# Kernel tuning notes

Hardware: AMD Instinct MI355X
Metric: run time of the kernel (lower is better)

## Reference

```python
import jax, jax.numpy as jnp
import numpy as np

B, H, W, C = 2, 48, 96, 128
N = H * W
NH, HD = 8, 32
WIN_R = 1
WLEN = 2 * WIN_R + 2
ATTN_NUM = WLEN * WLEN
FIELD_DIM = 2
D_SELF = C + FIELD_DIM + NH * 2   # 146
E_SELF = D_SELF + 1               # 147 (noc embed)
D_CROSS = C + FIELD_DIM           # 130
ATTN_DIM = NH * HD                # 256
HID = C * 2                       # ConvGLU hidden
SCALE = HD ** -0.5


def init_coords():
    gx, gy = jnp.meshgrid(jnp.arange(W, dtype=jnp.float32), jnp.arange(H, dtype=jnp.float32))
    return jnp.stack([gx, gy], axis=-1)[None]  # [1,H,W,2] (x,y)


def layer_norm(x, g, b, eps=1e-5):
    mu = x.mean(-1, keepdims=True)
    var = ((x - mu) ** 2).mean(-1, keepdims=True)
    return (x - mu) * jax.lax.rsqrt(var + eps) * g + b


def swap_halves(t):
    a, b = jnp.split(t, 2, axis=0)
    return jnp.concatenate([b, a], axis=0)


def bilinear_sample(img, coords):
    # img [B,H,W,C]; coords [B,H,W,2] absolute (x,y)
    x = jnp.clip(coords[..., 0], 0.0, W - 1.0)
    y = jnp.clip(coords[..., 1], 0.0, H - 1.0)
    x0 = jnp.clip(jnp.floor(x), 0, W - 2).astype(jnp.int32); x1 = x0 + 1
    y0 = jnp.clip(jnp.floor(y), 0, H - 2).astype(jnp.int32); y1 = y0 + 1
    wx = (x - x0)[..., None]; wy = (y - y0)[..., None]
    bi = jnp.arange(img.shape[0])[:, None, None]
    v00 = img[bi, y0, x0]; v01 = img[bi, y0, x1]
    v10 = img[bi, y1, x0]; v11 = img[bi, y1, x1]
    return (1 - wy) * ((1 - wx) * v00 + wx * v01) + wy * ((1 - wx) * v10 + wx * v11)


def consistency_mask(field, A=2.0):
    offset = field + init_coords()
    f_t2r = bilinear_sample(swap_halves(field), offset)
    diff = jnp.abs(field + f_t2r).sum(-1, keepdims=True)
    return (diff < A).astype(field.dtype)  # [B,H,W,1]


def match_attention_core(q, k, v, max_offset):
    # q,k,v: [B,N,NH,HD]; max_offset: [B,N,NH,2] absolute (x,y)
    r = WIN_R
    ox = jnp.clip(max_offset[..., 0], float(r), W - 1 - r - 0.001)
    oy = jnp.clip(max_offset[..., 1], float(r), H - 1 - r - 0.001)
    mxf = jnp.floor(ox); myf = jnp.floor(oy)
    fx = (ox - mxf).transpose(0, 2, 1)[..., None, None]  # [B,NH,N,1,1]
    fy = (oy - myf).transpose(0, 2, 1)[..., None, None]
    mx = mxf.astype(jnp.int32).transpose(0, 2, 1)  # [B,NH,N]
    my = myf.astype(jnp.int32).transpose(0, 2, 1)
    qh = q.transpose(0, 2, 1, 3); kh = k.transpose(0, 2, 1, 3); vh = v.transpose(0, 2, 1, 3)
    dxs = jnp.arange(WLEN) - r                    # window: floor-r .. floor+r+1
    gx = mx[..., None] + dxs                      # [B,NH,N,WLEN]
    gy = my[..., None] + dxs
    idx = (gy[..., :, None] * W + gx[..., None, :]).reshape(B, NH, N, ATTN_NUM)
    bi = jnp.arange(B)[:, None, None, None]
    hi = jnp.arange(NH)[None, :, None, None]
    kg = kh[bi, hi, idx]                          # [B,NH,N,ATTN_NUM,HD]
    s = jnp.einsum('bhnd,bhnad->bhna', qh, kg) * SCALE
    S = s.reshape(B, NH, N, WLEN, WLEN)           # [..., y, x]
    w00 = (1 - fy) * (1 - fx); w01 = (1 - fy) * fx; w10 = fy * (1 - fx); w11 = fy * fx
    # continuous (2r+1)^2 window scores by bilinear interp of integer-grid scores
    s_cont = (w00 * S[..., :-1, :-1] + w01 * S[..., :-1, 1:]
              + w10 * S[..., 1:, :-1] + w11 * S[..., 1:, 1:])
    p = jax.nn.softmax(s_cont.reshape(B, NH, N, -1), axis=-1).reshape(s_cont.shape)
    # scatter continuous probs back to the (2r+2)^2 integer grid with bilinear weights
    Ag = jnp.zeros((B, NH, N, WLEN, WLEN), p.dtype)
    Ag = Ag.at[..., :-1, :-1].add(w00 * p)
    Ag = Ag.at[..., :-1, 1:].add(w01 * p)
    Ag = Ag.at[..., 1:, :-1].add(w10 * p)
    Ag = Ag.at[..., 1:, 1:].add(w11 * p)
    Af = Ag.reshape(B, NH, N, ATTN_NUM)
    vg = vh[bi, hi, idx]                          # [B,NH,N,ATTN_NUM,HD]
    out = jnp.einsum('bhna,bhnad->bhnd', Af, vg)
    return out.transpose(0, 2, 1, 3).reshape(B, N, ATTN_DIM), Af.transpose(0, 2, 1, 3)


def reference(x, self_rpos, field, field_scale, n0_g, n0_b, n1_g, n1_b, n2_g, n2_b,
              sq_w, sk_w, sv_w, sp_w, cq_w, ck_w, cv_w, cg_w, cp_w,
              fc1_w, fc1_b, dw_w, dw_b, fc2_w, fc2_b):
    noc = consistency_mask(jax.lax.stop_gradient(field))
    xc = jnp.concatenate([x, field * field_scale, self_rpos], axis=-1)  # [B,H,W,D_SELF]
    coords0 = jnp.tile(init_coords(), (1, 1, 1, NH))  # [1,H,W,2*NH]
    self_off = (self_rpos + coords0).reshape(B, N, NH, 2)
    # --- self MatchAttention (noc_embed) ---
    h0 = layer_norm(xc, n0_g, n0_b).reshape(B, N, D_SELF)
    xe = jnp.concatenate([h0, noc.reshape(B, N, 1)], axis=-1)
    q = (xe @ sq_w).reshape(B, N, NH, HD)
    k = (xe @ sk_w).reshape(B, N, NH, HD)
    v = (xe @ sv_w).reshape(B, N, NH, HD)
    o, _ = match_attention_core(q, k, v, self_off)
    xc = xc + (o @ sp_w).reshape(B, H, W, D_SELF)
    self_rpos_out = xc[..., -NH * 2:]
    xc = xc[..., :D_CROSS]
    xc = xc.at[..., -1].set(0.0)  # stereo: zero y-flow
    field1 = xc[..., -FIELD_DIM:] / field_scale
    off = (jnp.tile(field1, (1, 1, 1, NH)) + coords0).reshape(B, N, NH, 2)
    # --- cross MatchAttention ---
    h1 = layer_norm(xc, n1_g, n1_b).reshape(B, N, D_CROSS)
    ref = h1
    tgt = swap_halves(h1)
    g = jax.nn.silu(ref @ cg_w)
    q = (ref @ cq_w).reshape(B, N, NH, HD)
    k = (tgt @ ck_w).reshape(B, N, NH, HD)
    v = (tgt @ cv_w).reshape(B, N, NH, HD)
    o, attn = match_attention_core(q, k, v, off)
    o = jnp.concatenate([g * o, attn.reshape(B, N, NH * ATTN_NUM)], axis=-1)
    xc = xc + (o @ cp_w).reshape(B, H, W, D_CROSS)
    xc = xc.at[..., -1].set(0.0)
    field2 = xc[..., -FIELD_DIM:] / field_scale
    xo = xc[..., :C]
    # --- ConvGLU MLP ---
    h2 = layer_norm(xo, n2_g, n2_b)
    u = h2 @ fc1_w + fc1_b
    a, gv = jnp.split(u, 2, axis=-1)
    a = jax.lax.conv_general_dilated(a, dw_w, (1, 1), 'SAME',
                                     dimension_numbers=('NHWC', 'HWIO', 'NHWC'),
                                     feature_group_count=HID) + dw_b
    a = jax.nn.gelu(a, approximate=False) * gv
    xo = xo + (a @ fc2_w + fc2_b)
    return xo, self_rpos_out, field2


def setup_inputs() -> dict:
    key = jax.random.key(0)
    ks = jax.random.split(key, 16)
    def rn(i, shape, s=1.0):
        return jax.random.normal(ks[i], shape, dtype=jnp.float32) * s
    return {
        'x': rn(0, (B, H, W, C)),
        'self_rpos': rn(1, (B, H, W, NH * 2)),
        'field': rn(2, (B, H, W, FIELD_DIM)),
        'field_scale': 0.1 * jnp.ones((1, 1, 1, 2), jnp.float32),
        'n0_g': jnp.ones((D_SELF,), jnp.float32), 'n0_b': jnp.zeros((D_SELF,), jnp.float32),
        'n1_g': jnp.ones((D_CROSS,), jnp.float32), 'n1_b': jnp.zeros((D_CROSS,), jnp.float32),
        'n2_g': jnp.ones((C,), jnp.float32), 'n2_b': jnp.zeros((C,), jnp.float32),
        'sq_w': rn(3, (E_SELF, ATTN_DIM), 0.02), 'sk_w': rn(4, (E_SELF, ATTN_DIM), 0.02),
        'sv_w': rn(5, (E_SELF, ATTN_DIM), 0.02), 'sp_w': rn(6, (ATTN_DIM, D_SELF), 0.02),
        'cq_w': rn(7, (D_CROSS, ATTN_DIM), 0.02), 'ck_w': rn(8, (D_CROSS, ATTN_DIM), 0.02),
        'cv_w': rn(9, (D_CROSS, ATTN_DIM), 0.02), 'cg_w': rn(10, (D_CROSS, ATTN_DIM), 0.02),
        'cp_w': rn(11, (ATTN_DIM + NH * ATTN_NUM, D_CROSS), 0.02),
        'fc1_w': rn(12, (C, 2 * HID), 0.02), 'fc1_b': jnp.zeros((2 * HID,), jnp.float32),
        'dw_w': rn(13, (3, 3, 1, HID), 0.1), 'dw_b': jnp.zeros((HID,), jnp.float32),
        'fc2_w': rn(14, (HID, C), 0.02), 'fc2_b': jnp.zeros((C,), jnp.float32),
    }
```

## Files before the change

### kernel.cpp

```cpp
#include <hip/hip_runtime.h>
#include <math.h>

namespace {
constexpr int Bn = 2, Hh = 48, Ww = 96, Cch = 128;
constexpr int Nn = Hh * Ww;
constexpr int NHh = 8;
constexpr int DSELF = 146, ESELF = 147, DCROSS = 130;
constexpr int Mrows = Bn * Nn;
constexpr float SCALEf = 0.17677669529663687f;
}

typedef float f32x4 __attribute__((ext_vector_type(4)));
typedef short s16x8 __attribute__((ext_vector_type(8)));

__device__ __forceinline__ unsigned short f2b(float f) {
  unsigned int u = __float_as_uint(f);
  u = u + 0x7fffu + ((u >> 16) & 1u);
  return (unsigned short)(u >> 16);
}

__device__ __forceinline__ f32x4 mfma_bf16(s16x8 a, s16x8 b, f32x4 c) {
  f32x4 d;
  asm volatile("v_mfma_f32_16x16x32_bf16 %0, %1, %2, %3"
               : "=&v"(d) : "v"(a), "v"(b), "v"(c));
  return d;
}

__device__ __forceinline__ float wave_bcast_sum(float v) {
#pragma unroll
  for (int off = 32; off > 0; off >>= 1) v += __shfl_down(v, off);
  return __shfl(v, 0);
}

struct WDesc { const float* src; int K, N, Kp, dstOff, blkOff; };
struct WPack { WDesc d[11]; };

__global__ __launch_bounds__(256) void convert_w_kernel(WPack p, unsigned short* dst) {
  int bi = blockIdx.x;
  int mi = 0;
#pragma unroll
  for (int i = 1; i < 11; i++) if (bi >= p.d[i].blkOff) mi = i;
  WDesc w = p.d[mi];
  int e = (bi - w.blkOff) * 2048 + threadIdx.x * 8;
  int total = w.N * w.Kp;
  if (e >= total) return;
  int n = e / w.Kp, k0 = e - n * w.Kp;
  s16x8 pack;
#pragma unroll
  for (int j = 0; j < 8; j++) {
    int kk = k0 + j;
    float vv = (kk < w.K) ? w.src[(size_t)kk * w.N + n] : 0.f;
    pack[j] = (short)f2b(vv);
  }
  *reinterpret_cast<s16x8*>(dst + w.dstOff + e) = pack;
}

__global__ __launch_bounds__(256) void mfma_gemm_kernel(
    const unsigned short* __restrict__ A, int Kp,
    const unsigned short* __restrict__ Wt, int N,
    const float* __restrict__ bias, const float* __restrict__ resid,
    float* __restrict__ out, int swapA, int act) {
  __shared__ unsigned short As[64 * 40];
  __shared__ unsigned short Bs[64 * 40];
  int tid = threadIdx.x;
  int m0 = blockIdx.y * 64, n0 = blockIdx.x * 64;
  int lane = tid & 63, wv = tid >> 6;
  int wr = wv >> 1, wc = wv & 1;
  int lr = lane & 15, lk = (lane >> 4) * 8;
  int sr = tid >> 2, sk8 = (tid & 3) * 8;
  int am = m0 + sr;
  if (swapA) am = (am < Mrows / 2) ? am + Mrows / 2 : am - Mrows / 2;
  const unsigned short* aptr = A + (size_t)am * Kp + sk8;
  int bn = n0 + sr;
  const unsigned short* bptr = (bn < N) ? Wt + (size_t)bn * Kp + sk8 : nullptr;
  f32x4 acc00 = {}, acc01 = {}, acc10 = {}, acc11 = {};
  for (int k0 = 0; k0 < Kp; k0 += 32) {
    s16x8 av = *reinterpret_cast<const s16x8*>(aptr + k0);
    s16x8 bv = {};
    if (bptr) bv = *reinterpret_cast<const s16x8*>(bptr + k0);
    *reinterpret_cast<s16x8*>(&As[sr * 40 + sk8]) = av;
    *reinterpret_cast<s16x8*>(&Bs[sr * 40 + sk8]) = bv;
    __syncthreads();
    s16x8 a0 = *reinterpret_cast<const s16x8*>(&As[(wr * 32 + lr) * 40 + lk]);
    s16x8 a1 = *reinterpret_cast<const s16x8*>(&As[(wr * 32 + 16 + lr) * 40 + lk]);
    s16x8 b0 = *reinterpret_cast<const s16x8*>(&Bs[(wc * 32 + lr) * 40 + lk]);
    s16x8 b1 = *reinterpret_cast<const s16x8*>(&Bs[(wc * 32 + 16 + lr) * 40 + lk]);
    acc00 = mfma_bf16(a0, b0, acc00);
    acc01 = mfma_bf16(a0, b1, acc01);
    acc10 = mfma_bf16(a1, b0, acc10);
    acc11 = mfma_bf16(a1, b1, acc11);
    __syncthreads();
  }
  int rowBase = m0 + wr * 32 + (lane >> 4) * 4;
  f32x4 accs[2][2] = {{acc00, acc01}, {acc10, acc11}};
#pragma unroll
  for (int fc = 0; fc < 2; fc++) {
    int col = n0 + wc * 32 + fc * 16 + lr;
    if (col >= N) continue;
    float bval = bias ? bias[col] : 0.f;
#pragma unroll
    for (int fr = 0; fr < 2; fr++) {
#pragma unroll
      for (int r = 0; r < 4; r++) {
        int row = rowBase + fr * 16 + r;
        float vv = accs[fr][fc][r] + bval;
        if (resid) vv += resid[(size_t)row * N + col];
        if (act == 1) vv = vv / (1.f + expf(-vv));
        out[(size_t)row * N + col] = vv;
      }
    }
  }
}

__global__ __launch_bounds__(256) void prep_kernel(
    const float* __restrict__ x, const float* __restrict__ rpos,
    const float* __restrict__ field, const float* __restrict__ fs,
    const float* __restrict__ n0g, const float* __restrict__ n0b,
    float* __restrict__ xc, unsigned short* __restrict__ xe_b) {
  int wv = threadIdx.x >> 6, lane = threadIdx.x & 63;
  int pix = blockIdx.x * 4 + wv;
  int b = pix / Nn, n = pix - b * Nn;
  int py = n / Ww, px = n - py * Ww;
  const float* xrow = x + (size_t)pix * Cch;
  const float* rrow = rpos + (size_t)pix * 16;
  float f0 = field[(size_t)pix * 2 + 0], f1 = field[(size_t)pix * 2 + 1];
  float fsx = fs[0], fsy = fs[1];
  float vals[3];
#pragma unroll
  for (int i = 0; i < 3; i++) {
    int c = lane + i * 64;
    float v = 0.f;
    if (c < Cch) v = xrow[c];
    else if (c == 128) v = f0 * fsx;
    else if (c == 129) v = f1 * fsy;
    else if (c < DSELF) v = rrow[c - 130];
    vals[i] = v;
  }
  float* xcrow = xc + (size_t)pix * DSELF;
#pragma unroll
  for (int i = 0; i < 3; i++) {
    int c = lane + i * 64;
    if (c < DSELF) xcrow[c] = vals[i];
  }
  float s = 0.f;
#pragma unroll
  for (int i = 0; i < 3; i++) { int c = lane + i * 64; if (c < DSELF) s += vals[i]; }
  float mu = wave_bcast_sum(s) * (1.f / DSELF);
  float s2 = 0.f;
#pragma unroll
  for (int i = 0; i < 3; i++) {
    int c = lane + i * 64;
    if (c < DSELF) { float d = vals[i] - mu; s2 += d * d; }
  }
  float var = wave_bcast_sum(s2) * (1.f / DSELF);
  float rs = rsqrtf(var + 1e-5f);
  float noc = 0.f;
  if (lane == 0) {
    float ox = fminf(fmaxf(f0 + (float)px, 0.f), (float)(Ww - 1));
    float oy = fminf(fmaxf(f1 + (float)py, 0.f), (float)(Hh - 1));
    float x0f = fminf(fmaxf(floorf(ox), 0.f), (float)(Ww - 2));
    float y0f = fminf(fmaxf(floorf(oy), 0.f), (float)(Hh - 2));
    int x0 = (int)x0f, y0 = (int)y0f;
    float wx = ox - x0f, wy = oy - y0f;
    const float* fo = field + (size_t)(1 - b) * Nn * 2;
    const float* p00 = fo + ((size_t)y0 * Ww + x0) * 2;
    const float* p10 = fo + ((size_t)(y0 + 1) * Ww + x0) * 2;
    float v0 = (1.f - wy) * ((1.f - wx) * p00[0] + wx * p00[2]) +
               wy * ((1.f - wx) * p10[0] + wx * p10[2]);
    float v1 = (1.f - wy) * ((1.f - wx) * p00[1] + wx * p00[3]) +
               wy * ((1.f - wx) * p10[1] + wx * p10[3]);
    float diff = fabsf(f0 + v0) + fabsf(f1 + v1);
    noc = (diff < 2.f) ? 1.f : 0.f;
  }
  noc = __shfl(noc, 0);
  unsigned short* xerow = xe_b + (size_t)pix * 160;
#pragma unroll
  for (int i = 0; i < 3; i++) {
    int c = lane + i * 64;
    if (c < 160) {
      float v;
      if (c < DSELF) v = (vals[i] - mu) * rs * n0g[c] + n0b[c];
      else if (c == 146) v = noc;
      else v = 0.f;
      xerow[c] = f2b(v);
    }
  }
}

__global__ __launch_bounds__(256) void attn_wave_kernel(
    const float* __restrict__ q, const float* __restrict__ k,
    const float* __restrict__ v, const float* __restrict__ rpos,
    const float* __restrict__ xc2, const float* __restrict__ fs,
    const float* __restrict__ g, unsigned short* __restrict__ o, int o_stride,
    int mode) {
  int wv = threadIdx.x >> 6, lane = threadIdx.x & 63;
  int pix = blockIdx.x * 4 + wv;
  int b = pix / Nn, n = pix - b * Nn;
  int py = n / Ww, px = n - py * Ww;
  int h = lane >> 3, c = lane & 7;
  size_t row = (size_t)pix;
  float ox, oy;
  if (mode == 0) {
    ox = rpos[row * 16 + 2 * h] + (float)px;
    oy = rpos[row * 16 + 2 * h + 1] + (float)py;
  } else {
    ox = xc2[row * DCROSS + 128] / fs[0] + (float)px;
    oy = (float)py;
  }
  ox = fminf(fmaxf(ox, 1.0f), 93.999f);
  oy = fminf(fmaxf(oy, 1.0f), 45.999f);
  float mxf = floorf(ox), myf = floorf(oy);
  float fx = ox - mxf, fy = oy - myf;
  int mx = (int)mxf, my = (int)myf;
  int base = b * Nn;

  float4 qv = *reinterpret_cast<const float4*>(q + row * 256 + lane * 4);
  float s[16];
#pragma unroll
  for (int j = 0; j < 4; j++) {
    int gy = my - 1 + j;
#pragma unroll
    for (int i = 0; i < 4; i++) {
      int gx = mx - 1 + i;
      int idx = gy * Ww + gx;
      float4 kv = *reinterpret_cast<const float4*>(
          k + (size_t)(base + idx) * 256 + lane * 4);
      float d = qv.x * kv.x + qv.y * kv.y + qv.z * kv.z + qv.w * kv.w;
      d += __shfl_xor(d, 1);
      d += __shfl_xor(d, 2);
      d += __shfl_xor(d, 4);
      s[j * 4 + i] = d * SCALEf;
    }
  }
  float w00 = (1.f - fy) * (1.f - fx), w01 = (1.f - fy) * fx;
  float w10 = fy * (1.f - fx), w11 = fy * fx;
  float sc[9];
#pragma unroll
  for (int j = 0; j < 3; j++)
#pragma unroll
    for (int i = 0; i < 3; i++)
      sc[j * 3 + i] = w00 * s[j * 4 + i] + w01 * s[j * 4 + i + 1] +
                      w10 * s[(j + 1) * 4 + i] + w11 * s[(j + 1) * 4 + i + 1];
  float mval = sc[0];
#pragma unroll
  for (int i = 1; i < 9; i++) mval = fmaxf(mval, sc[i]);
  float p[9], psum = 0.f;
#pragma unroll
  for (int i = 0; i < 9; i++) { p[i] = expf(sc[i] - mval); psum += p[i]; }
  float inv = 1.f / psum;
#pragma unroll
  for (int i = 0; i < 9; i++) p[i] *= inv;
  float Ag[16] = {};
#pragma unroll
  for (int j = 0; j < 3; j++)
#pragma unroll
    for (int i = 0; i < 3; i++) {
      float pv = p[j * 3 + i];
      Ag[j * 4 + i] += w00 * pv;
      Ag[j * 4 + i + 1] += w01 * pv;
      Ag[(j + 1) * 4 + i] += w10 * pv;
      Ag[(j + 1) * 4 + i + 1] += w11 * pv;
    }
  float4 acc = make_float4(0.f, 0.f, 0.f, 0.f);
#pragma unroll
  for (int j = 0; j < 4; j++) {
    int gy = my - 1 + j;
#pragma unroll
    for (int i = 0; i < 4; i++) {
      int gx = mx - 1 + i;
      int idx = gy * Ww + gx;
      float4 vv = *reinterpret_cast<const float4*>(
          v + (size_t)(base + idx) * 256 + lane * 4);
      float w = Ag[j * 4 + i];
      acc.x += w * vv.x; acc.y += w * vv.y; acc.z += w * vv.z; acc.w += w * vv.w;
    }
  }
  if (g) {
    float4 gg = *reinterpret_cast<const float4*>(g + row * 256 + lane * 4);
    acc.x *= gg.x; acc.y *= gg.y; acc.z *= gg.z; acc.w *= gg.w;
  }
  unsigned int p0 = (unsigned int)f2b(acc.x) | ((unsigned int)f2b(acc.y) << 16);
  unsigned int p1 = (unsigned int)f2b(acc.z) | ((unsigned int)f2b(acc.w) << 16);
  *reinterpret_cast<uint2*>(o + row * o_stride + lane * 4) = make_uint2(p0, p1);
  if (mode == 1) {
    float a0 = 0.f, a1 = 0.f;
#pragma unroll
    for (int a = 0; a < 8; a++) {
      if (c == a) { a0 = Ag[2 * a]; a1 = Ag[2 * a + 1]; }
    }
    unsigned int pa = (unsigned int)f2b(a0) | ((unsigned int)f2b(a1) << 16);
    *reinterpret_cast<unsigned int*>(o + row * o_stride + 256 + h * 16 + 2 * c) = pa;
  }
}

__global__ __launch_bounds__(256) void post_self_kernel(
    const float* __restrict__ xcn, const float* __restrict__ n1g,
    const float* __restrict__ n1b, float* __restrict__ out_rpos,
    float* __restrict__ xc2, unsigned short* __restrict__ h1_b) {
  int wv = threadIdx.x >> 6, lane = threadIdx.x & 63;
  int pix = blockIdx.x * 4 + wv;
  const float* row = xcn + (size_t)pix * DSELF;
  float vals[3];
#pragma unroll
  for (int i = 0; i < 3; i++) {
    int c = lane + i * 64;
    vals[i] = (c < DSELF) ? row[c] : 0.f;
  }
#pragma unroll
  for (int i = 0; i < 3; i++) {
    int c = lane + i * 64;
    if (c >= 130 && c < 146) out_rpos[(size_t)pix * 16 + (c - 130)] = vals[i];
  }
#pragma unroll
  for (int i = 0; i < 3; i++) {
    int c = lane + i * 64;
    if (c == 129) vals[i] = 0.f;
  }
  float* x2row = xc2 + (size_t)pix * DCROSS;
#pragma unroll
  for (int i = 0; i < 3; i++) {
    int c = lane + i * 64;
    if (c < DCROSS) x2row[c] = vals[i];
  }
  float s = 0.f;
#pragma unroll
  for (int i = 0; i < 3; i++) { int c = lane + i * 64; if (c < DCROSS) s += vals[i]; }
  float mu = wave_bcast_sum(s) * (1.f / DCROSS);
  float s2 = 0.f;
#pragma unroll
  for (int i = 0; i < 3; i++) {
    int c = lane + i * 64;
    if (c < DCROSS) { float d = vals[i] - mu; s2 += d * d; }
  }
  float var = wave_bcast_sum(s2) * (1.f / DCROSS);
  float rs = rsqrtf(var + 1e-5f);
  unsigned short* h1row = h1_b + (size_t)pix * 160;
#pragma unroll
  for (int i = 0; i < 3; i++) {
    int c = lane + i * 64;
    if (c < 160) {
      float v = (c < DCROSS) ? (vals[i] - mu) * rs * n1g[c] + n1b[c] : 0.f;
      h1row[c] = f2b(v);
    }
  }
}

__global__ __launch_bounds__(256) void post_cross_kernel(
    const float* __restrict__ xc2n, const float* __restrict__ fs,
    const float* __restrict__ n2g, const float* __restrict__ n2b,
    float* __restrict__ out_f2, float* __restrict__ xob,
    unsigned short* __restrict__ h2_b) {
  int wv = threadIdx.x >> 6, lane = threadIdx.x & 63;
  int pix = blockIdx.x * 4 + wv;
  const float* row = xc2n + (size_t)pix * DCROSS;
  float vals[3];
#pragma unroll
  for (int i = 0; i < 3; i++) {
    int c = lane + i * 64;
    vals[i] = (c < DCROSS) ? row[c] : 0.f;
  }
  if (lane == 0) out_f2[(size_t)pix * 2 + 0] = vals[2] / fs[0];
  if (lane == 1) out_f2[(size_t)pix * 2 + 1] = 0.f;
  float* xrow = xob + (size_t)pix * Cch;
#pragma unroll
  for (int i = 0; i < 2; i++) {
    int c = lane + i * 64;
    xrow[c] = vals[i];
  }
  float s = vals[0] + vals[1];
  float mu = wave_bcast_sum(s) * (1.f / Cch);
  float d0 = vals[0] - mu, d1 = vals[1] - mu;
  float var = wave_bcast_sum(d0 * d0 + d1 * d1) * (1.f / Cch);
  float rs = rsqrtf(var + 1e-5f);
  unsigned short* h2row = h2_b + (size_t)pix * Cch;
#pragma unroll
  for (int i = 0; i < 2; i++) {
    int c = lane + i * 64;
    h2row[c] = f2b((vals[i] - mu) * rs * n2g[c] + n2b[c]);
  }
}

__global__ __launch_bounds__(256) void dwconv_kernel(
    const float* __restrict__ u, const float* __restrict__ dww,
    const float* __restrict__ dwb, unsigned short* __restrict__ aout) {
  int t = blockIdx.x * 256 + threadIdx.x;
  int c = t & 255;
  int pix = t >> 8;
  int b = pix / Nn, n = pix - b * Nn;
  int py = n / Ww, px = n - py * Ww;
  float acc = dwb[c];
#pragma unroll
  for (int ky = 0; ky < 3; ky++) {
    int yy = py + ky - 1;
    if (yy < 0 || yy >= Hh) continue;
#pragma unroll
    for (int kx = 0; kx < 3; kx++) {
      int xx = px + kx - 1;
      if (xx < 0 || xx >= Ww) continue;
      acc += u[((size_t)(b * Nn + yy * Ww + xx)) * 512 + c] * dww[(ky * 3 + kx) * 256 + c];
    }
  }
  float ge = 0.5f * acc * (1.f + erff(acc * 0.70710678118654752f));
  aout[(size_t)pix * 256 + c] = f2b(ge * u[(size_t)pix * 512 + 256 + c]);
}

extern "C" void kernel_launch(void* const* d_in, const int* in_sizes, int n_in,
                              void* d_out, int out_size, void* d_ws, size_t ws_size,
                              hipStream_t stream) {
  (void)in_sizes; (void)n_in; (void)out_size; (void)ws_size;
  const float* x    = (const float*)d_in[0];
  const float* rpos = (const float*)d_in[1];
  const float* field= (const float*)d_in[2];
  const float* fs   = (const float*)d_in[3];
  const float* n0g  = (const float*)d_in[4];
  const float* n0b  = (const float*)d_in[5];
  const float* n1g  = (const float*)d_in[6];
  const float* n1b  = (const float*)d_in[7];
  const float* n2g  = (const float*)d_in[8];
  const float* n2b  = (const float*)d_in[9];
  const float* sq_w = (const float*)d_in[10];
  const float* sk_w = (const float*)d_in[11];
  const float* sv_w = (const float*)d_in[12];
  const float* sp_w = (const float*)d_in[13];
  const float* cq_w = (const float*)d_in[14];
  const float* ck_w = (const float*)d_in[15];
  const float* cv_w = (const float*)d_in[16];
  const float* cg_w = (const float*)d_in[17];
  const float* cp_w = (const float*)d_in[18];
  const float* fc1w = (const float*)d_in[19];
  const float* fc1b = (const float*)d_in[20];
  const float* dww  = (const float*)d_in[21];
  const float* dwb  = (const float*)d_in[22];
  const float* fc2w = (const float*)d_in[23];
  const float* fc2b = (const float*)d_in[24];

  float* ws = (float*)d_ws;
  float* xc   = ws + 0;
  float* xcn  = ws + 1345536;
  float* q    = ws + 2691072;
  float* k    = ws + 5050368;
  float* v    = ws + 7409664;
  float* g    = ws + 9768960;
  float* xc2  = ws + 12128256;
  float* xob  = ws + 13326336;
  unsigned short* xe_b   = (unsigned short*)(ws + 14505984);
  unsigned short* o_b    = (unsigned short*)(ws + 15243264);
  unsigned short* h1_b   = (unsigned short*)(ws + 16422912);
  unsigned short* ocat_b = (unsigned short*)(ws + 17160192);
  unsigned short* h2_b   = (unsigned short*)(ws + 18929664);
  unsigned short* warena = (unsigned short*)(ws + 19519488);
  float* u    = q;
  float* xc2n = v;
  unsigned short* aconv_b = o_b;

  float* out_xo   = (float*)d_out;
  float* out_rpos = out_xo + 1179648;
  float* out_f2   = out_xo + 1327104;

  const int oSQ = 0, oSK = 40960, oSV = 81920, oSP = 122880, oCQ = 160256,
            oCK = 201216, oCV = 242176, oCG = 283136, oCP = 324096,
            oF1 = 374016, oF2 = 439552;
  WPack wp;
  auto setw = [&](int i, const float* src, int K, int N, int Kp, int off) {
    wp.d[i].src = src; wp.d[i].K = K; wp.d[i].N = N; wp.d[i].Kp = Kp;
    wp.d[i].dstOff = off;
  };
  setw(0, sq_w, 147, 256, 160, oSQ);
  setw(1, sk_w, 147, 256, 160, oSK);
  setw(2, sv_w, 147, 256, 160, oSV);
  setw(3, sp_w, 256, 146, 256, oSP);
  setw(4, cq_w, 130, 256, 160, oCQ);
  setw(5, ck_w, 130, 256, 160, oCK);
  setw(6, cv_w, 130, 256, 160, oCV);
  setw(7, cg_w, 130, 256, 160, oCG);
  setw(8, cp_w, 384, 130, 384, oCP);
  setw(9, fc1w, 128, 512, 128, oF1);
  setw(10, fc2w, 256, 128, 256, oF2);
  int nblk = 0;
  for (int i = 0; i < 11; i++) {
    wp.d[i].blkOff = nblk;
    nblk += (wp.d[i].N * wp.d[i].Kp + 2047) / 2048;
  }

  dim3 blk(256);
  auto gemm = [&](const unsigned short* A, int Kp, int woff, int N,
                  const float* bias, const float* resid, float* out,
                  int swapA, int act) {
    dim3 grid((N + 63) / 64, Mrows / 64);
    mfma_gemm_kernel<<<grid, blk, 0, stream>>>(A, Kp, warena + woff, N, bias,
                                               resid, out, swapA, act);
  };

  convert_w_kernel<<<nblk, blk, 0, stream>>>(wp, warena);
  prep_kernel<<<2304, blk, 0, stream>>>(x, rpos, field, fs, n0g, n0b, xc, xe_b);
  gemm(xe_b, 160, oSQ, 256, nullptr, nullptr, q, 0, 0);
  gemm(xe_b, 160, oSK, 256, nullptr, nullptr, k, 0, 0);
  gemm(xe_b, 160, oSV, 256, nullptr, nullptr, v, 0, 0);
  attn_wave_kernel<<<2304, blk, 0, stream>>>(q, k, v, rpos, nullptr, fs, nullptr,
                                             o_b, 256, 0);
  gemm(o_b, 256, oSP, 146, nullptr, xc, xcn, 0, 0);
  post_self_kernel<<<2304, blk, 0, stream>>>(xcn, n1g, n1b, out_rpos, xc2, h1_b);
  gemm(h1_b, 160, oCQ, 256, nullptr, nullptr, q, 0, 0);
  gemm(h1_b, 160, oCK, 256, nullptr, nullptr, k, 1, 0);
  gemm(h1_b, 160, oCV, 256, nullptr, nullptr, v, 1, 0);
  gemm(h1_b, 160, oCG, 256, nullptr, nullptr, g, 0, 1);
  attn_wave_kernel<<<2304, blk, 0, stream>>>(q, k, v, nullptr, xc2, fs, g,
                                             ocat_b, 384, 1);
  gemm(ocat_b, 384, oCP, 130, nullptr, xc2, xc2n, 0, 0);
  post_cross_kernel<<<2304, blk, 0, stream>>>(xc2n, fs, n2g, n2b, out_f2, xob, h2_b);
  gemm(h2_b, 128, oF1, 512, fc1b, nullptr, u, 0, 0);
  dwconv_kernel<<<9216, blk, 0, stream>>>(u, dww, dwb, aconv_b);
  gemm(aconv_b, 256, oF2, 128, fc2b, xob, out_xo, 0, 0);
}
```

Measured before the change: 182.8 us.

## Fuse QKV and cross projections into wide GEMMs, store FFN hidden as bf16

Packs the self-attention Q/K/V weights into one contiguous block and runs a single N=768 GEMM. The cross Q+G and K+V projections become two N=512 GEMMs, with SiLU applied only to the gate columns. The attention kernel now reads q/k/v/g through strides and offsets into these interleaved buffers. The fc1 output is written as bf16, and the depthwise conv is vectorised to process 8 channels per thread from that bf16 buffer. This cuts kernel launches and halves the memory traffic of the FFN intermediate, at the cost of bf16 rounding on the hidden activations and larger attention read strides.

```diff
diff --git a/kernel.cpp b/kernel.cpp
--- a/kernel.cpp
+++ b/kernel.cpp
@@ -18,6 +18,9 @@
   u = u + 0x7fffu + ((u >> 16) & 1u);
   return (unsigned short)(u >> 16);
 }
+__device__ __forceinline__ float b2f(unsigned short u) {
+  return __uint_as_float((unsigned int)u << 16);
+}
 
 __device__ __forceinline__ f32x4 mfma_bf16(s16x8 a, s16x8 b, f32x4 c) {
   f32x4 d;
@@ -59,7 +62,7 @@
     const unsigned short* __restrict__ A, int Kp,
     const unsigned short* __restrict__ Wt, int N,
     const float* __restrict__ bias, const float* __restrict__ resid,
-    float* __restrict__ out, int swapA, int act) {
+    void* __restrict__ out, int swapA, int act, int out_bf16) {
   __shared__ unsigned short As[64 * 40];
   __shared__ unsigned short Bs[64 * 40];
   int tid = threadIdx.x;
@@ -98,6 +101,7 @@
     int col = n0 + wc * 32 + fc * 16 + lr;
     if (col >= N) continue;
     float bval = bias ? bias[col] : 0.f;
+    bool dosilu = (act == 1) || (act == 2 && col >= 256);
 #pragma unroll
     for (int fr = 0; fr < 2; fr++) {
 #pragma unroll
@@ -105,8 +109,11 @@
         int row = rowBase + fr * 16 + r;
         float vv = accs[fr][fc][r] + bval;
         if (resid) vv += resid[(size_t)row * N + col];
-        if (act == 1) vv = vv / (1.f + expf(-vv));
-        out[(size_t)row * N + col] = vv;
+        if (dosilu) vv = vv / (1.f + expf(-vv));
+        if (out_bf16)
+          ((unsigned short*)out)[(size_t)row * N + col] = f2b(vv);
+        else
+          ((float*)out)[(size_t)row * N + col] = vv;
       }
     }
   }
@@ -188,10 +195,10 @@
 }
 
 __global__ __launch_bounds__(256) void attn_wave_kernel(
-    const float* __restrict__ q, const float* __restrict__ k,
-    const float* __restrict__ v, const float* __restrict__ rpos,
-    const float* __restrict__ xc2, const float* __restrict__ fs,
-    const float* __restrict__ g, unsigned short* __restrict__ o, int o_stride,
+    const float* __restrict__ qbuf, int qstride, int gOff,
+    const float* __restrict__ kvbuf, int kvstride, int koff, int voff,
+    const float* __restrict__ rpos, const float* __restrict__ xc2,
+    const float* __restrict__ fs, unsigned short* __restrict__ o, int o_stride,
     int mode) {
   int wv = threadIdx.x >> 6, lane = threadIdx.x & 63;
   int pix = blockIdx.x * 4 + wv;
@@ -214,7 +221,7 @@
   int mx = (int)mxf, my = (int)myf;
   int base = b * Nn;
 
-  float4 qv = *reinterpret_cast<const float4*>(q + row * 256 + lane * 4);
+  float4 qv = *reinterpret_cast<const float4*>(qbuf + row * qstride + lane * 4);
   float s[16];
 #pragma unroll
   for (int j = 0; j < 4; j++) {
@@ -224,7 +231,7 @@
       int gx = mx - 1 + i;
       int idx = gy * Ww + gx;
       float4 kv = *reinterpret_cast<const float4*>(
-          k + (size_t)(base + idx) * 256 + lane * 4);
+          kvbuf + (size_t)(base + idx) * kvstride + koff + lane * 4);
       float d = qv.x * kv.x + qv.y * kv.y + qv.z * kv.z + qv.w * kv.w;
       d += __shfl_xor(d, 1);
       d += __shfl_xor(d, 2);
@@ -270,13 +277,13 @@
       int gx = mx - 1 + i;
       int idx = gy * Ww + gx;
       float4 vv = *reinterpret_cast<const float4*>(
-          v + (size_t)(base + idx) * 256 + lane * 4);
+          kvbuf + (size_t)(base + idx) * kvstride + voff + lane * 4);
       float w = Ag[j * 4 + i];
       acc.x += w * vv.x; acc.y += w * vv.y; acc.z += w * vv.z; acc.w += w * vv.w;
     }
   }
-  if (g) {
-    float4 gg = *reinterpret_cast<const float4*>(g + row * 256 + lane * 4);
+  if (gOff >= 0) {
+    float4 gg = *reinterpret_cast<const float4*>(qbuf + row * qstride + gOff + lane * 4);
     acc.x *= gg.x; acc.y *= gg.y; acc.z *= gg.z; acc.w *= gg.w;
   }
   unsigned int p0 = (unsigned int)f2b(acc.x) | ((unsigned int)f2b(acc.y) << 16);
@@ -381,14 +388,16 @@
 }
 
 __global__ __launch_bounds__(256) void dwconv_kernel(
-    const float* __restrict__ u, const float* __restrict__ dww,
+    const unsigned short* __restrict__ ub, const float* __restrict__ dww,
     const float* __restrict__ dwb, unsigned short* __restrict__ aout) {
   int t = blockIdx.x * 256 + threadIdx.x;
-  int c = t & 255;
-  int pix = t >> 8;
+  int c8 = (t & 31) * 8;
+  int pix = t >> 5;
   int b = pix / Nn, n = pix - b * Nn;
   int py = n / Ww, px = n - py * Ww;
-  float acc = dwb[c];
+  float acc[8];
+#pragma unroll
+  for (int j = 0; j < 8; j++) acc[j] = dwb[c8 + j];
 #pragma unroll
   for (int ky = 0; ky < 3; ky++) {
     int yy = py + ky - 1;
@@ -397,11 +406,23 @@
     for (int kx = 0; kx < 3; kx++) {
       int xx = px + kx - 1;
       if (xx < 0 || xx >= Ww) continue;
-      acc += u[((size_t)(b * Nn + yy * Ww + xx)) * 512 + c] * dww[(ky * 3 + kx) * 256 + c];
-    }
-  }
-  float ge = 0.5f * acc * (1.f + erff(acc * 0.70710678118654752f));
-  aout[(size_t)pix * 256 + c] = f2b(ge * u[(size_t)pix * 512 + 256 + c]);
+      s16x8 uv = *reinterpret_cast<const s16x8*>(
+          ub + ((size_t)(b * Nn + yy * Ww + xx)) * 512 + c8);
+      const float* wrow = dww + (ky * 3 + kx) * 256 + c8;
+#pragma unroll
+      for (int j = 0; j < 8; j++)
+        acc[j] += b2f((unsigned short)uv[j]) * wrow[j];
+    }
+  }
+  s16x8 gate = *reinterpret_cast<const s16x8*>(ub + (size_t)pix * 512 + 256 + c8);
+  s16x8 outp;
+#pragma unroll
+  for (int j = 0; j < 8; j++) {
+    float a = acc[j];
+    float ge = 0.5f * a * (1.f + erff(a * 0.70710678118654752f));
+    outp[j] = (short)f2b(ge * b2f((unsigned short)gate[j]));
+  }
+  *reinterpret_cast<s16x8*>(aout + (size_t)pix * 256 + c8) = outp;
 }
 
 extern "C" void kernel_launch(void* const* d_in, const int* in_sizes, int n_in,
@@ -435,44 +456,47 @@
   const float* fc2b = (const float*)d_in[24];
 
   float* ws = (float*)d_ws;
-  float* xc   = ws + 0;
-  float* xcn  = ws + 1345536;
-  float* q    = ws + 2691072;
-  float* k    = ws + 5050368;
-  float* v    = ws + 7409664;
-  float* g    = ws + 9768960;
-  float* xc2  = ws + 12128256;
-  float* xob  = ws + 13326336;
-  unsigned short* xe_b   = (unsigned short*)(ws + 14505984);
-  unsigned short* o_b    = (unsigned short*)(ws + 15243264);
-  unsigned short* h1_b   = (unsigned short*)(ws + 16422912);
-  unsigned short* ocat_b = (unsigned short*)(ws + 17160192);
-  unsigned short* h2_b   = (unsigned short*)(ws + 18929664);
-  unsigned short* warena = (unsigned short*)(ws + 19519488);
-  float* u    = q;
-  float* xc2n = v;
+  float* xc    = ws + 0;
+  float* xcn   = ws + 1345536;
+  float* xc2   = ws + 2691072;
+  float* xc2n  = ws + 3889152;
+  float* xob   = ws + 5087232;
+  unsigned short* xe_b   = (unsigned short*)(ws + 6266880);
+  unsigned short* h1_b   = (unsigned short*)(ws + 7004160);
+  unsigned short* h2_b   = (unsigned short*)(ws + 7741440);
+  float* qkv   = ws + 8331264;
+  float* qg    = ws + 15409152;
+  float* kv    = ws + 20127744;
+  unsigned short* o_b    = (unsigned short*)(ws + 24846336);
+  unsigned short* ocat_b = (unsigned short*)(ws + 26025984);
+  unsigned short* warena = (unsigned short*)(ws + 27795456);
+  unsigned short* u_b    = (unsigned short*)qkv;
   unsigned short* aconv_b = o_b;
 
   float* out_xo   = (float*)d_out;
   float* out_rpos = out_xo + 1179648;
   float* out_f2   = out_xo + 1327104;
 
-  const int oSQ = 0, oSK = 40960, oSV = 81920, oSP = 122880, oCQ = 160256,
-            oCK = 201216, oCV = 242176, oCG = 283136, oCP = 324096,
-            oF1 = 374016, oF2 = 439552;
+  const int oSQKV = 0;
+  const int oSP   = 122880;
+  const int oCQG  = 160256;
+  const int oCKV  = 242176;
+  const int oCP   = 324096;
+  const int oF1   = 374016;
+  const int oF2   = 439552;
   WPack wp;
   auto setw = [&](int i, const float* src, int K, int N, int Kp, int off) {
     wp.d[i].src = src; wp.d[i].K = K; wp.d[i].N = N; wp.d[i].Kp = Kp;
     wp.d[i].dstOff = off;
   };
-  setw(0, sq_w, 147, 256, 160, oSQ);
-  setw(1, sk_w, 147, 256, 160, oSK);
-  setw(2, sv_w, 147, 256, 160, oSV);
+  setw(0, sq_w, 147, 256, 160, oSQKV);
+  setw(1, sk_w, 147, 256, 160, oSQKV + 40960);
+  setw(2, sv_w, 147, 256, 160, oSQKV + 81920);
   setw(3, sp_w, 256, 146, 256, oSP);
-  setw(4, cq_w, 130, 256, 160, oCQ);
-  setw(5, ck_w, 130, 256, 160, oCK);
-  setw(6, cv_w, 130, 256, 160, oCV);
-  setw(7, cg_w, 130, 256, 160, oCG);
+  setw(4, cq_w, 130, 256, 160, oCQG);
+  setw(5, cg_w, 130, 256, 160, oCQG + 40960);
+  setw(6, ck_w, 130, 256, 160, oCKV);
+  setw(7, cv_w, 130, 256, 160, oCKV + 40960);
   setw(8, cp_w, 384, 130, 384, oCP);
   setw(9, fc1w, 128, 512, 128, oF1);
   setw(10, fc2w, 256, 128, 256, oF2);
@@ -484,31 +508,27 @@
 
   dim3 blk(256);
   auto gemm = [&](const unsigned short* A, int Kp, int woff, int N,
-                  const float* bias, const float* resid, float* out,
-                  int swapA, int act) {
+                  const float* bias, const float* resid, void* out,
+                  int swapA, int act, int obf) {
     dim3 grid((N + 63) / 64, Mrows / 64);
     mfma_gemm_kernel<<<grid, blk, 0, stream>>>(A, Kp, warena + woff, N, bias,
-                                               resid, out, swapA, act);
+                                               resid, out, swapA, act, obf);
   };
 
   convert_w_kernel<<<nblk, blk, 0, stream>>>(wp, warena);
   prep_kernel<<<2304, blk, 0, stream>>>(x, rpos, field, fs, n0g, n0b, xc, xe_b);
-  gemm(xe_b, 160, oSQ, 256, nullptr, nullptr, q, 0, 0);
-  gemm(xe_b, 160, oSK, 256, nullptr, nullptr, k, 0, 0);
-  gemm(xe_b, 160, oSV, 256, nullptr, nullptr, v, 0, 0);
-  attn_wave_kernel<<<2304, blk, 0, stream>>>(q, k, v, rpos, nullptr, fs, nullptr,
-                                             o_b, 256, 0);
-  gemm(o_b, 256, oSP, 146, nullptr, xc, xcn, 0, 0);
+  gemm(xe_b, 160, oSQKV, 768, nullptr, nullptr, qkv, 0, 0, 0);
+  attn_wave_kernel<<<2304, blk, 0, stream>>>(qkv, 768, -1, qkv, 768, 256, 512,
+                                             rpos, nullptr, fs, o_b, 256, 0);
+  gemm(o_b, 256, oSP, 146, nullptr, xc, xcn, 0, 0, 0);
   post_self_kernel<<<2304, blk, 0, stream>>>(xcn, n1g, n1b, out_rpos, xc2, h1_b);
-  gemm(h1_b, 160, oCQ, 256, nullptr, nullptr, q, 0, 0);
-  gemm(h1_b, 160, oCK, 256, nullptr, nullptr, k, 1, 0);
-  gemm(h1_b, 160, oCV, 256, nullptr, nullptr, v, 1, 0);
-  gemm(h1_b, 160, oCG, 256, nullptr, nullptr, g, 0, 1);
-  attn_wave_kernel<<<2304, blk, 0, stream>>>(q, k, v, nullptr, xc2, fs, g,
-                                             ocat_b, 384, 1);
-  gemm(ocat_b, 384, oCP, 130, nullptr, xc2, xc2n, 0, 0);
+  gemm(h1_b, 160, oCQG, 512, nullptr, nullptr, qg, 0, 2, 0);
+  gemm(h1_b, 160, oCKV, 512, nullptr, nullptr, kv, 1, 0, 0);
+  attn_wave_kernel<<<2304, blk, 0, stream>>>(qg, 512, 256, kv, 512, 0, 256,
+                                             nullptr, xc2, fs, ocat_b, 384, 1);
+  gemm(ocat_b, 384, oCP, 130, nullptr, xc2, xc2n, 0, 0, 0);
   post_cross_kernel<<<2304, blk, 0, stream>>>(xc2n, fs, n2g, n2b, out_f2, xob, h2_b);
-  gemm(h2_b, 128, oF1, 512, fc1b, nullptr, u, 0, 0);
-  dwconv_kernel<<<9216, blk, 0, stream>>>(u, dww, dwb, aconv_b);
-  gemm(aconv_b, 256, oF2, 128, fc2b, xob, out_xo, 0, 0);
-}
+  gemm(h2_b, 128, oF1, 512, fc1b, nullptr, u_b, 0, 0, 1);
+  dwconv_kernel<<<1152, blk, 0, stream>>>(u_b, dww, dwb, aconv_b);
+  gemm(aconv_b, 256, oF2, 128, fc2b, xob, out_xo, 0, 0, 0);
+}
```

After: 161.9 us. 1.13x faster.
